# Kernel tuning notes

Hardware: AMD Instinct MI355X
Metric: run time of the kernel (lower is better)

Reference implementation:

```python
import jax, jax.numpy as jnp
import numpy as np

N_PER_GRAPH = 468
B = 32
N = B * N_PER_GRAPH            # 14976 nodes
E = 89600                      # synthetic Delaunay-like directed edges
IN_DIM, HID, OUT, HEADS = 2, 256, 512, 4
NEG_SLOPE = 0.2
EPS = 1e-16


def setup_inputs() -> dict:
    key = jax.random.key(0)
    ks = jax.random.split(key, 12)
    x = jax.random.uniform(ks[0], (N, IN_DIM), dtype=jnp.float32)
    edge_index = jax.random.randint(ks[1], (2, E), 0, N, dtype=jnp.int64)
    batch = jnp.repeat(jnp.arange(B, dtype=jnp.int64), N_PER_GRAPH)
    s1 = 1.0 / np.sqrt(IN_DIM)
    s2 = 1.0 / np.sqrt(HID)
    sg = 1.0 / np.sqrt(OUT)
    return {
        "x": x,
        "edge_index": edge_index,
        "batch": batch,
        # GATConv 1: in_dim -> hidden, heads=4, concat=False
        "W1": jax.random.normal(ks[2], (IN_DIM, HEADS * HID), jnp.float32) * s1,
        "a1_src": jax.random.normal(ks[3], (HEADS, HID), jnp.float32) * s2,
        "a1_dst": jax.random.normal(ks[4], (HEADS, HID), jnp.float32) * s2,
        "b1": jnp.zeros((HID,), jnp.float32),
        # GATConv 2: hidden -> out, heads=4, concat=False
        "W2": jax.random.normal(ks[5], (HID, HEADS * OUT), jnp.float32) * s2,
        "a2_src": jax.random.normal(ks[6], (HEADS, OUT), jnp.float32) * sg,
        "a2_dst": jax.random.normal(ks[7], (HEADS, OUT), jnp.float32) * sg,
        "b2": jnp.zeros((OUT,), jnp.float32),
        # GlobalAttention gate_nn: Linear(out_dim, 1)
        "Wg": jax.random.normal(ks[8], (OUT, 1), jnp.float32) * sg,
        "bg": jnp.zeros((1,), jnp.float32),
    }


def _gat_layer(x, src, dst, W, a_src, a_dst, b, heads, out_ch):
    n = x.shape[0]
    xh = (x @ W).reshape(n, heads, out_ch)            # [N,H,C]
    alpha_s = jnp.einsum("nhc,hc->nh", xh, a_src)     # [N,H]
    alpha_d = jnp.einsum("nhc,hc->nh", xh, a_dst)
    e = alpha_s[src] + alpha_d[dst]                   # [E,H]
    e = jnp.where(e > 0, e, NEG_SLOPE * e)            # leaky_relu(0.2)
    # segment softmax over incoming edges of each destination node
    m = jax.ops.segment_max(e, dst, num_segments=n)
    ex = jnp.exp(e - m[dst])
    denom = jax.ops.segment_sum(ex, dst, num_segments=n)
    alpha = ex / (denom[dst] + EPS)                   # [E,H]
    msg = xh[src] * alpha[:, :, None]                 # [E,H,C]
    out = jax.ops.segment_sum(msg, dst, num_segments=n)  # [N,H,C]
    return out.mean(axis=1) + b                       # concat=False -> head mean


def reference(x, edge_index, batch, W1, a1_src, a1_dst, b1,
              W2, a2_src, a2_dst, b2, Wg, bg):
    n = x.shape[0]
    # PyG GATConv default add_self_loops=True (both layers use the same graph)
    loops = jnp.arange(n, dtype=edge_index.dtype)
    src = jnp.concatenate([edge_index[0], loops])
    dst = jnp.concatenate([edge_index[1], loops])

    h = _gat_layer(x, src, dst, W1, a1_src, a1_dst, b1, HEADS, HID)
    h = jax.nn.relu(h)
    h = _gat_layer(h, src, dst, W2, a2_src, a2_dst, b2, HEADS, OUT)
    h = jax.nn.relu(h)

    # GlobalAttention pooling: gate = Linear(out,1), softmax per graph, weighted sum
    gate = h @ Wg + bg                                # [N,1]
    gm = jax.ops.segment_max(gate, batch, num_segments=B)
    ge = jnp.exp(gate - gm[batch])
    gs = jax.ops.segment_sum(ge, batch, num_segments=B)
    attn = ge / (gs[batch] + EPS)                     # [N,1]
    pooled = jax.ops.segment_sum(attn * h, batch, num_segments=B)  # [B,512]
    return pooled.reshape(-1, 1, OUT)                 # [B,1,512]
```

## Files before the change

kernel.cpp:

```cpp
#include <hip/hip_runtime.h>
#include <hip/hip_bf16.h>
#include <math.h>

#define HEADS 4
#define C1 256
#define C2 512
#define NEG 0.2f
#define EPSF 1e-16f

using bf16x8 = __attribute__((ext_vector_type(8))) short;
using f32x4  = __attribute__((ext_vector_type(4))) float;

__device__ __forceinline__ float lrelu(float e) { return e > 0.f ? e : NEG * e; }

__device__ __forceinline__ unsigned short f2bf(float v) {
    __hip_bfloat16 b = __float2bfloat16(v);
    return *reinterpret_cast<unsigned short*>(&b);
}
__device__ __forceinline__ float bf2f(unsigned short u) {
    __hip_bfloat16 b = *reinterpret_cast<__hip_bfloat16*>(&u);
    return __bfloat162float(b);
}


__global__ __launch_bounds__(256) void k1_prep_deg(
    const float* __restrict__ W1, const float* __restrict__ a1s, const float* __restrict__ a1d,
    const float* __restrict__ W2, const float* __restrict__ a2s, const float* __restrict__ a2d,
    const int* __restrict__ ei, int E,
    float* __restrict__ w1a, float* __restrict__ w2a,
    unsigned short* __restrict__ W2t_hi, unsigned short* __restrict__ W2t_lo,
    int* __restrict__ deg)
{
    int b = blockIdx.x, tid = threadIdx.x;
    int wv = tid >> 6, lane = tid & 63;
    if (b == 0) {
#pragma unroll
        for (int q = 0; q < 4; q++) {
            int o = wv * 4 + q, sd = o >> 3, idx = o & 7, h = idx >> 1, d = idx & 1;
            const float* av = sd ? a1d : a1s;
            float p = 0.f;
            for (int c = lane; c < 256; c += 64) p += W1[d * 1024 + h * 256 + c] * av[h * 256 + c];
#pragma unroll
            for (int m = 32; m >= 1; m >>= 1) p += __shfl_xor(p, m, 64);
            if (lane == 0) w1a[o] = p;
        }
    } else if (b <= 8) {
        int bb = b - 1, sd = bb >> 2, h = bb & 3;
        const float* av = sd ? a2d : a2s;
        float gv[8];
#pragma unroll
        for (int q = 0; q < 8; q++) gv[q] = av[h * 512 + lane * 8 + q];
        for (int k = wv; k < 256; k += 4) {
            const float4 w0 = *reinterpret_cast<const float4*>(&W2[(size_t)k * 2048 + h * 512 + lane * 8]);
            const float4 w1 = *reinterpret_cast<const float4*>(&W2[(size_t)k * 2048 + h * 512 + lane * 8 + 4]);
            float p = w0.x*gv[0] + w0.y*gv[1] + w0.z*gv[2] + w0.w*gv[3]
                    + w1.x*gv[4] + w1.y*gv[5] + w1.z*gv[6] + w1.w*gv[7];
#pragma unroll
            for (int m = 32; m >= 1; m >>= 1) p += __shfl_xor(p, m, 64);
            if (lane == 0) w2a[sd * 1024 + h * 256 + k] = p;
        }
    } else if (b <= 136) {
        __shared__ float T[64][65];
        int lin = b - 9;
        int kk0 = (lin & 15) * 64, n0 = (lin >> 4) * 64;
        int h = kk0 >> 8, k0 = kk0 & 255;
#pragma unroll
        for (int rr = 0; rr < 16; rr++) {
            int ki = rr * 4 + (tid >> 6), ni = tid & 63;
            T[ki][ni] = W2[(size_t)(k0 + ki) * 2048 + h * 512 + n0 + ni];
        }
        __syncthreads();
#pragma unroll
        for (int rr = 0; rr < 16; rr++) {
            int ni = rr * 4 + (tid >> 6), ki = tid & 63;
            float v = T[ki][ni];
            unsigned short hi = f2bf(v);
            unsigned short lo = f2bf(v - bf2f(hi));
            size_t o = (size_t)(n0 + ni) * 1024 + kk0 + ki;
            W2t_hi[o] = hi; W2t_lo[o] = lo;
        }
    } else {
        int i = (b - 137) * 256 + tid;
        if (i < E) atomicAdd(&deg[ei[E + i]], 1);
    }
}

__global__ __launch_bounds__(1024) void k2_node1_scan(
    const float* __restrict__ x, const float* __restrict__ w1a,
    float* __restrict__ as1, float* __restrict__ ad1, int N,
    const int* __restrict__ deg, int* __restrict__ row_ptr, int* __restrict__ cursor)
{
    int b = blockIdx.x, tid = threadIdx.x;
    if (b < 15) {
        int n = b * 1024 + tid;
        if (n >= N) return;
        float x0 = x[2 * n], x1 = x[2 * n + 1];
        float4 av, dv;
        float* ap = &av.x; float* dp = &dv.x;
#pragma unroll
        for (int h = 0; h < 4; h++) {
            ap[h] = x0 * w1a[h * 2] + x1 * w1a[h * 2 + 1];
            dp[h] = x0 * w1a[8 + h * 2] + x1 * w1a[8 + h * 2 + 1];
        }
        *reinterpret_cast<float4*>(&as1[n * 4]) = av;
        *reinterpret_cast<float4*>(&ad1[n * 4]) = dv;
    } else {
        __shared__ int sd[1024];
        int per = (N + 1023) >> 10;
        int vals[24];
        int start = tid * per, local = 0;
        for (int i = 0; i < per && i < 24; i++) {
            int idx = start + i;
            int d = (idx < N) ? deg[idx] : 0;
            vals[i] = d; local += d;
        }
        sd[tid] = local; __syncthreads();
        for (int off = 1; off < 1024; off <<= 1) {
            int v = sd[tid];
            int a = (tid >= off) ? sd[tid - off] : 0;
            __syncthreads();
            sd[tid] = v + a;
            __syncthreads();
        }
        int run = (tid > 0) ? sd[tid - 1] : 0;
        for (int i = 0; i < per && i < 24; i++) {
            int idx = start + i;
            if (idx < N) { row_ptr[idx] = run; cursor[idx] = run; run += vals[i]; }
        }
        if (tid == 1023) row_ptr[N] = sd[1023];
    }
}

__global__ void k3_scatter(const int* __restrict__ ei, int E,
                           int* __restrict__ cursor, int* __restrict__ csr_src)
{
    int i = blockIdx.x * blockDim.x + threadIdx.x;
    if (i >= E) return;
    int s = ei[i], d = ei[E + i];
    int pos = atomicAdd(&cursor[d], 1);
    csr_src[pos] = s;
}

__global__ __launch_bounds__(256) void k4_agg1_h1(
    const float* __restrict__ x, const float* __restrict__ as1, const float* __restrict__ ad1,
    const int* __restrict__ row_ptr, const int* __restrict__ csr_src,
    const float* __restrict__ W1, const float* __restrict__ b1, const float* __restrict__ w2a,
    float* __restrict__ h1, float* __restrict__ as2, float* __restrict__ ad2)
{
    int wv = threadIdx.x >> 6, lane = threadIdx.x & 63;
    int n = blockIdx.x * 4 + wv;
    const float4 sa4 = *reinterpret_cast<const float4*>(&as1[n * 4]);
    const float4 da4 = *reinterpret_cast<const float4*>(&ad1[n * 4]);
    const float sa[4] = {sa4.x, sa4.y, sa4.z, sa4.w};
    const float da[4] = {da4.x, da4.y, da4.z, da4.w};
    float acc[8] = {0,0,0,0,0,0,0,0};
    float den[4] = {0,0,0,0};
    int beg = row_ptr[n], end = row_ptr[n + 1];
    for (int e = beg + lane; e < end; e += 64) {
        int s = csr_src[e];
        const float4 a4 = *reinterpret_cast<const float4*>(&as1[s * 4]);
        const float af[4] = {a4.x, a4.y, a4.z, a4.w};
        const float2 xv = reinterpret_cast<const float2*>(x)[s];
#pragma unroll
        for (int q = 0; q < 4; q++) {
            float w = expf(lrelu(af[q] + da[q]));
            den[q] += w;
            acc[2 * q]     = fmaf(w, xv.x, acc[2 * q]);
            acc[2 * q + 1] = fmaf(w, xv.y, acc[2 * q + 1]);
        }
    }
#pragma unroll
    for (int msk = 1; msk <= 32; msk <<= 1) {
#pragma unroll
        for (int q = 0; q < 8; q++) acc[q] += __shfl_xor(acc[q], msk, 64);
#pragma unroll
        for (int q = 0; q < 4; q++) den[q] += __shfl_xor(den[q], msk, 64);
    }
    const float2 xn = reinterpret_cast<const float2*>(x)[n];
    float xa[8];
#pragma unroll
    for (int q = 0; q < 4; q++) {
        float ws = expf(lrelu(sa[q] + da[q]));
        float dq = den[q] + ws;
        float inv = 1.f / (dq + EPSF);
        xa[2 * q]     = (acc[2 * q]     + ws * xn.x) * inv;
        xa[2 * q + 1] = (acc[2 * q + 1] + ws * xn.y) * inv;
    }
    float v[4];
#pragma unroll
    for (int q = 0; q < 4; q++) {
        int c = lane * 4 + q;
        float t = 0.f;
#pragma unroll
        for (int h = 0; h < 4; h++)
#pragma unroll
            for (int d = 0; d < 2; d++)
                t = fmaf(xa[h * 2 + d], W1[d * 1024 + h * 256 + c], t);
        v[q] = fmaxf(fmaf(0.25f, t, b1[c]), 0.f);
    }
    *reinterpret_cast<float4*>(&h1[(size_t)n * 256 + lane * 4]) = make_float4(v[0], v[1], v[2], v[3]);
    float p[8];
#pragma unroll
    for (int o = 0; o < 8; o++) {
        int sd = o >> 2, h = o & 3;
        float t = 0.f;
#pragma unroll
        for (int q = 0; q < 4; q++) t = fmaf(v[q], w2a[sd * 1024 + h * 256 + lane * 4 + q], t);
        p[o] = t;
    }
#pragma unroll
    for (int msk = 1; msk <= 32; msk <<= 1)
#pragma unroll
        for (int o = 0; o < 8; o++) p[o] += __shfl_xor(p[o], msk, 64);
    if (lane == 0) {
        *reinterpret_cast<float4*>(&as2[n * 4]) = make_float4(p[0], p[1], p[2], p[3]);
        *reinterpret_cast<float4*>(&ad2[n * 4]) = make_float4(p[4], p[5], p[6], p[7]);
    }
}

__global__ __launch_bounds__(256) void k6_agg2(
    const float* __restrict__ h1, const float* __restrict__ as2, const float* __restrict__ ad2,
    const int* __restrict__ row_ptr, const int* __restrict__ csr_src,
    unsigned short* __restrict__ hagg_hi, unsigned short* __restrict__ hagg_lo)
{
    int wv = threadIdx.x >> 6, lane = threadIdx.x & 63;
    int n = blockIdx.x * 4 + wv;
    const float4 sa4 = *reinterpret_cast<const float4*>(&as2[n * 4]);
    const float4 da4 = *reinterpret_cast<const float4*>(&ad2[n * 4]);
    const float sa[4] = {sa4.x, sa4.y, sa4.z, sa4.w};
    const float da[4] = {da4.x, da4.y, da4.z, da4.w};
    float den[4], acc[4][4];
    const float4 hs = *reinterpret_cast<const float4*>(&h1[(size_t)n * 256 + lane * 4]);
    const float hv0[4] = {hs.x, hs.y, hs.z, hs.w};
#pragma unroll
    for (int h = 0; h < 4; h++) {
        float ws = expf(lrelu(sa[h] + da[h]));
        den[h] = ws;
#pragma unroll
        for (int q = 0; q < 4; q++) acc[h][q] = ws * hv0[q];
    }
    int beg = row_ptr[n], end = row_ptr[n + 1];
    for (int e = beg; e < end; e++) {
        int s = csr_src[e];
        const float4 a4 = *reinterpret_cast<const float4*>(&as2[s * 4]);
        const float af[4] = {a4.x, a4.y, a4.z, a4.w};
        const float4 hv = *reinterpret_cast<const float4*>(&h1[(size_t)s * 256 + lane * 4]);
#pragma unroll
        for (int h = 0; h < 4; h++) {
            float w = expf(lrelu(af[h] + da[h]));
            den[h] += w;
            acc[h][0] = fmaf(w, hv.x, acc[h][0]);
            acc[h][1] = fmaf(w, hv.y, acc[h][1]);
            acc[h][2] = fmaf(w, hv.z, acc[h][2]);
            acc[h][3] = fmaf(w, hv.w, acc[h][3]);
        }
    }
#pragma unroll
    for (int h = 0; h < 4; h++) {
        float inv = 1.f / (den[h] + EPSF);
        ushort4 hi4, lo4;
        unsigned short* hp = &hi4.x; unsigned short* lp = &lo4.x;
#pragma unroll
        for (int q = 0; q < 4; q++) {
            float val = acc[h][q] * inv;
            unsigned short hi = f2bf(val);
            hp[q] = hi;
            lp[q] = f2bf(val - bf2f(hi));
        }
        size_t o = (size_t)n * 1024 + h * 256 + lane * 4;
        *reinterpret_cast<ushort4*>(&hagg_hi[o]) = hi4;
        *reinterpret_cast<ushort4*>(&hagg_lo[o]) = lo4;
    }
}

__global__ __launch_bounds__(256) void k7_gemm2(
    const unsigned short* __restrict__ Ahi, const unsigned short* __restrict__ Alo,
    const unsigned short* __restrict__ Bhi, const unsigned short* __restrict__ Blo,
    const float* __restrict__ b2, const float* __restrict__ Wg,
    float* __restrict__ h2, float* __restrict__ gate)
{
    __shared__ __align__(16) unsigned short As_hi[128 * 40], As_lo[128 * 40];
    __shared__ __align__(16) unsigned short Bs_hi[64 * 40],  Bs_lo[64 * 40];
    __shared__ float s_gate[128];
    int tid = threadIdx.x, l = tid & 63, wv = tid >> 6;
    int wr = wv >> 1, wc = wv & 1;
    int bid = blockIdx.x, rtile, ctile;
    if (bid < 896) { int g = bid >> 6, rem = bid & 63; rtile = g * 8 + (rem & 7); ctile = rem >> 3; }
    else           { int t = bid - 896; rtile = 112 + (t >> 3); ctile = t & 7; }
    int row0 = rtile * 128, col0 = ctile * 64;
    int lm = l & 15, lg = l >> 4;
    if (tid < 128) s_gate[tid] = 0.f;

    int ra0 = tid >> 2, ka0 = (tid & 3) * 8;
    int ra1 = (tid + 256) >> 2, ka1 = ((tid + 256) & 3) * 8;
    int rb = tid >> 2, kb = (tid & 3) * 8;

    f32x4 acc[4][2];
#pragma unroll
    for (int i = 0; i < 4; i++)
#pragma unroll
        for (int j = 0; j < 2; j++) { acc[i][j][0]=0.f; acc[i][j][1]=0.f; acc[i][j][2]=0.f; acc[i][j][3]=0.f; }

    uint4 pah0, pah1, pal0, pal1, pbh, pbl;
    {
        size_t ga0 = (size_t)(row0 + ra0) * 1024 + ka0;
        size_t ga1 = (size_t)(row0 + ra1) * 1024 + ka1;
        size_t gb  = (size_t)(col0 + rb) * 1024 + kb;
        pah0 = *reinterpret_cast<const uint4*>(Ahi + ga0); pal0 = *reinterpret_cast<const uint4*>(Alo + ga0);
        pah1 = *reinterpret_cast<const uint4*>(Ahi + ga1); pal1 = *reinterpret_cast<const uint4*>(Alo + ga1);
        pbh  = *reinterpret_cast<const uint4*>(Bhi + gb);  pbl  = *reinterpret_cast<const uint4*>(Blo + gb);
    }

    for (int kt = 0; kt < 1024; kt += 32) {
        *reinterpret_cast<uint4*>(&As_hi[ra0 * 40 + ka0]) = pah0;
        *reinterpret_cast<uint4*>(&As_lo[ra0 * 40 + ka0]) = pal0;
        *reinterpret_cast<uint4*>(&As_hi[ra1 * 40 + ka1]) = pah1;
        *reinterpret_cast<uint4*>(&As_lo[ra1 * 40 + ka1]) = pal1;
        *reinterpret_cast<uint4*>(&Bs_hi[rb * 40 + kb])   = pbh;
        *reinterpret_cast<uint4*>(&Bs_lo[rb * 40 + kb])   = pbl;
        __syncthreads();
        if (kt + 32 < 1024) {
            int ktn = kt + 32;
            size_t ga0 = (size_t)(row0 + ra0) * 1024 + ktn + ka0;
            size_t ga1 = (size_t)(row0 + ra1) * 1024 + ktn + ka1;
            size_t gb  = (size_t)(col0 + rb) * 1024 + ktn + kb;
            pah0 = *reinterpret_cast<const uint4*>(Ahi + ga0); pal0 = *reinterpret_cast<const uint4*>(Alo + ga0);
            pah1 = *reinterpret_cast<const uint4*>(Ahi + ga1); pal1 = *reinterpret_cast<const uint4*>(Alo + ga1);
            pbh  = *reinterpret_cast<const uint4*>(Bhi + gb);  pbl  = *reinterpret_cast<const uint4*>(Blo + gb);
        }
        bf16x8 ah[4], al[4], bh[2], bl[2];
#pragma unroll
        for (int i = 0; i < 4; i++) {
            int base = (wr * 64 + i * 16 + lm) * 40 + lg * 8;
            ah[i] = *reinterpret_cast<const bf16x8*>(&As_hi[base]);
            al[i] = *reinterpret_cast<const bf16x8*>(&As_lo[base]);
        }
#pragma unroll
        for (int j = 0; j < 2; j++) {
            int base = (wc * 32 + j * 16 + lm) * 40 + lg * 8;
            bh[j] = *reinterpret_cast<const bf16x8*>(&Bs_hi[base]);
            bl[j] = *reinterpret_cast<const bf16x8*>(&Bs_lo[base]);
        }
#pragma unroll
        for (int i = 0; i < 4; i++)
#pragma unroll
            for (int j = 0; j < 2; j++) {
                acc[i][j] = __builtin_amdgcn_mfma_f32_16x16x32_bf16(ah[i], bh[j], acc[i][j], 0, 0, 0);
                acc[i][j] = __builtin_amdgcn_mfma_f32_16x16x32_bf16(ah[i], bl[j], acc[i][j], 0, 0, 0);
                acc[i][j] = __builtin_amdgcn_mfma_f32_16x16x32_bf16(al[i], bh[j], acc[i][j], 0, 0, 0);
            }
        __syncthreads();
    }
    float b2c[2], wgj[2];
#pragma unroll
    for (int j = 0; j < 2; j++) {
        int col = col0 + wc * 32 + j * 16 + lm;
        b2c[j] = b2[col]; wgj[j] = Wg[col];
    }
#pragma unroll
    for (int i = 0; i < 4; i++) {
#pragma unroll
        for (int r = 0; r < 4; r++) {
            int row = row0 + wr * 64 + i * 16 + lg * 4 + r;
            float g = 0.f;
#pragma unroll
            for (int j = 0; j < 2; j++) {
                float v = fmaxf(fmaf(0.25f, acc[i][j][r], b2c[j]), 0.f);
                h2[(size_t)row * 512 + col0 + wc * 32 + j * 16 + lm] = v;
                g = fmaf(v, wgj[j], g);
            }
            g += __shfl_xor(g, 1, 64);
            g += __shfl_xor(g, 2, 64);
            g += __shfl_xor(g, 4, 64);
            g += __shfl_xor(g, 8, 64);
            if (lm == 0) atomicAdd(&s_gate[wr * 64 + i * 16 + lg * 4 + r], g);
        }
    }
    __syncthreads();
    if (tid < 128) atomicAdd(&gate[row0 + tid], s_gate[tid]);
}

__global__ __launch_bounds__(256) void k8a_stats(float* __restrict__ gate, int npg)
{
    int bq = blockIdx.x, tid = threadIdx.x;
    int n0 = bq * npg;
    __shared__ float s[256];
    float e0 = (tid < npg)       ? expf(gate[n0 + tid])       : 0.f;
    float e1 = (tid + 256 < npg) ? expf(gate[n0 + tid + 256]) : 0.f;
    s[tid] = e0 + e1; __syncthreads();
#pragma unroll
    for (int off = 128; off >= 1; off >>= 1) {
        if (tid < off) s[tid] += s[tid + off];
        __syncthreads();
    }
    float inv = 1.f / (s[0] + EPSF);
    if (tid < npg)       gate[n0 + tid]       = e0 * inv;
    if (tid + 256 < npg) gate[n0 + tid + 256] = e1 * inv;
}

__global__ __launch_bounds__(256) void k8b_pool(
    const float* __restrict__ attn, const float* __restrict__ h2,
    float* __restrict__ out, int npg, int nsplit)
{
    int bq = blockIdx.x, sp = blockIdx.y, tid = threadIdx.x;
    int slot = tid & 127, half = tid >> 7;
    int chunk = (npg + nsplit - 1) / nsplit;
    int i0 = sp * chunk, i1 = min(npg, i0 + chunk);
    int n0 = bq * npg;
    float4 acc = make_float4(0.f, 0.f, 0.f, 0.f);
    for (int i = i0 + half; i < i1; i += 2) {
        float w = attn[n0 + i];
        const float4 v = *reinterpret_cast<const float4*>(&h2[(size_t)(n0 + i) * 512 + slot * 4]);
        acc.x = fmaf(w, v.x, acc.x);
        acc.y = fmaf(w, v.y, acc.y);
        acc.z = fmaf(w, v.z, acc.z);
        acc.w = fmaf(w, v.w, acc.w);
    }
    __shared__ float4 sacc[128];
    if (half == 1) sacc[slot] = acc;
    __syncthreads();
    if (half == 0) {
        const float4 o = sacc[slot];
        float* op = &out[(size_t)bq * 512 + slot * 4];
        atomicAdd(op + 0, acc.x + o.x);
        atomicAdd(op + 1, acc.y + o.y);
        atomicAdd(op + 2, acc.z + o.z);
        atomicAdd(op + 3, acc.w + o.w);
    }
}

extern "C" void kernel_launch(void* const* d_in, const int* in_sizes, int n_in,
                              void* d_out, int out_size, void* d_ws, size_t ws_size,
                              hipStream_t stream)
{
    const float* x    = (const float*)d_in[0];
    const int*   ei   = (const int*)d_in[1];
    const float* W1   = (const float*)d_in[3];
    const float* a1s  = (const float*)d_in[4];
    const float* a1d  = (const float*)d_in[5];
    const float* b1   = (const float*)d_in[6];
    const float* W2   = (const float*)d_in[7];
    const float* a2s  = (const float*)d_in[8];
    const float* a2d  = (const float*)d_in[9];
    const float* b2   = (const float*)d_in[10];
    const float* Wg   = (const float*)d_in[11];
    float* out = (float*)d_out;

    const int N = in_sizes[0] / 2;
    const int E = in_sizes[1] / 2;
    const int Bq = out_size / C2;
    const int npg = N / Bq;

    char* w = (char*)d_ws;
    size_t off = 0;
    auto alloc = [&](size_t bytes) { void* p = w + off; off += (bytes + 255) & ~(size_t)255; return p; };

    float* h1       = (float*)alloc((size_t)N * 256 * 4);
    float* h2       = (float*)alloc((size_t)N * 512 * 4);
    unsigned short* hagg_hi = (unsigned short*)alloc((size_t)N * 1024 * 2);
    unsigned short* hagg_lo = (unsigned short*)alloc((size_t)N * 1024 * 2);
    unsigned short* W2t_hi  = (unsigned short*)alloc((size_t)512 * 1024 * 2);
    unsigned short* W2t_lo  = (unsigned short*)alloc((size_t)512 * 1024 * 2);
    float* as1   = (float*)alloc((size_t)N * 4 * 4);
    float* ad1   = (float*)alloc((size_t)N * 4 * 4);
    float* as2   = (float*)alloc((size_t)N * 4 * 4);
    float* ad2   = (float*)alloc((size_t)N * 4 * 4);
    int*   deg   = (int*)alloc((size_t)N * 4);
    float* gate  = (float*)alloc((size_t)N * 4);
    float* w1a   = (float*)alloc(16 * 4);
    float* w2a   = (float*)alloc(2048 * 4);
    int* row_ptr = (int*)alloc((size_t)(N + 1) * 4);
    int* cursor  = (int*)alloc((size_t)(N + 1) * 4);
    int* csr_src = (int*)alloc((size_t)E * 4);
    (void)ws_size; (void)n_in;

    const int EB = (E + 255) / 256;

    hipMemsetAsync(deg, 0, (size_t)N * 4 * 2, stream);
    hipMemsetAsync(out, 0, (size_t)out_size * 4, stream);

    k1_prep_deg<<<137 + EB, 256, 0, stream>>>(W1, a1s, a1d, W2, a2s, a2d, ei, E,
                                              w1a, w2a, W2t_hi, W2t_lo, deg);
    k2_node1_scan<<<16, 1024, 0, stream>>>(x, w1a, as1, ad1, N, deg, row_ptr, cursor);
    k3_scatter<<<EB, 256, 0, stream>>>(ei, E, cursor, csr_src);
    k4_agg1_h1<<<N / 4, 256, 0, stream>>>(x, as1, ad1, row_ptr, csr_src,
                                          W1, b1, w2a, h1, as2, ad2);
    k6_agg2<<<N / 4, 256, 0, stream>>>(h1, as2, ad2, row_ptr, csr_src, hagg_hi, hagg_lo);
    k7_gemm2<<<(N / 128) * 8, 256, 0, stream>>>(hagg_hi, hagg_lo, W2t_hi, W2t_lo,
                                                b2, Wg, h2, gate);
    k8a_stats<<<Bq, 256, 0, stream>>>(gate, npg);
    k8b_pool<<<dim3(Bq, 8), 256, 0, stream>>>(gate, h2, out, npg, 8);
}
```

Baseline: 281.1 us.

## Widen GEMM2 column tile to 128 and fuse pooling softmax with weighted sum

The second-layer GEMM now computes 128x128 output tiles per block instead of 128x64, so each A tile is loaded once for twice as many columns and the grid halves to 468 blocks. The gate softmax statistics and the attention-weighted pooling are merged into one kernel that writes outputs directly, which removes the output memset and the atomics. The larger tile doubles the accumulator registers and LDS use, which may lower occupancy, and the pooling kernel now launches fewer blocks.

```diff
diff --git a/kernel.cpp b/kernel.cpp
--- a/kernel.cpp
+++ b/kernel.cpp
@@ -280,55 +280,56 @@
     float* __restrict__ h2, float* __restrict__ gate)
 {
     __shared__ __align__(16) unsigned short As_hi[128 * 40], As_lo[128 * 40];
-    __shared__ __align__(16) unsigned short Bs_hi[64 * 40],  Bs_lo[64 * 40];
+    __shared__ __align__(16) unsigned short Bs_hi[128 * 40], Bs_lo[128 * 40];
     __shared__ float s_gate[128];
     int tid = threadIdx.x, l = tid & 63, wv = tid >> 6;
     int wr = wv >> 1, wc = wv & 1;
     int bid = blockIdx.x, rtile, ctile;
-    if (bid < 896) { int g = bid >> 6, rem = bid & 63; rtile = g * 8 + (rem & 7); ctile = rem >> 3; }
-    else           { int t = bid - 896; rtile = 112 + (t >> 3); ctile = t & 7; }
-    int row0 = rtile * 128, col0 = ctile * 64;
+    if (bid < 448) { rtile = (bid & 7) + 8 * (bid >> 5); ctile = (bid >> 3) & 3; }
+    else           { int t = bid - 448; rtile = 112 + (t >> 2); ctile = t & 3; }
+    int row0 = rtile * 128, col0 = ctile * 128;
     int lm = l & 15, lg = l >> 4;
     if (tid < 128) s_gate[tid] = 0.f;
 
-    int ra0 = tid >> 2, ka0 = (tid & 3) * 8;
-    int ra1 = (tid + 256) >> 2, ka1 = ((tid + 256) & 3) * 8;
-    int rb = tid >> 2, kb = (tid & 3) * 8;
-
-    f32x4 acc[4][2];
+    int r0 = tid >> 2, k00 = (tid & 3) * 8;
+    int r1 = (tid + 256) >> 2, k01 = ((tid + 256) & 3) * 8;
+
+    f32x4 acc[4][4];
 #pragma unroll
     for (int i = 0; i < 4; i++)
 #pragma unroll
-        for (int j = 0; j < 2; j++) { acc[i][j][0]=0.f; acc[i][j][1]=0.f; acc[i][j][2]=0.f; acc[i][j][3]=0.f; }
-
-    uint4 pah0, pah1, pal0, pal1, pbh, pbl;
+        for (int jj = 0; jj < 4; jj++) { acc[i][jj][0]=0.f; acc[i][jj][1]=0.f; acc[i][jj][2]=0.f; acc[i][jj][3]=0.f; }
+
+    uint4 pah0, pal0, pbh0, pbl0, pah1, pal1, pbh1, pbl1;
     {
-        size_t ga0 = (size_t)(row0 + ra0) * 1024 + ka0;
-        size_t ga1 = (size_t)(row0 + ra1) * 1024 + ka1;
-        size_t gb  = (size_t)(col0 + rb) * 1024 + kb;
+        size_t ga0 = (size_t)(row0 + r0) * 1024 + k00, gb0 = (size_t)(col0 + r0) * 1024 + k00;
+        size_t ga1 = (size_t)(row0 + r1) * 1024 + k01, gb1 = (size_t)(col0 + r1) * 1024 + k01;
         pah0 = *reinterpret_cast<const uint4*>(Ahi + ga0); pal0 = *reinterpret_cast<const uint4*>(Alo + ga0);
+        pbh0 = *reinterpret_cast<const uint4*>(Bhi + gb0); pbl0 = *reinterpret_cast<const uint4*>(Blo + gb0);
         pah1 = *reinterpret_cast<const uint4*>(Ahi + ga1); pal1 = *reinterpret_cast<const uint4*>(Alo + ga1);
-        pbh  = *reinterpret_cast<const uint4*>(Bhi + gb);  pbl  = *reinterpret_cast<const uint4*>(Blo + gb);
+        pbh1 = *reinterpret_cast<const uint4*>(Bhi + gb1); pbl1 = *reinterpret_cast<const uint4*>(Blo + gb1);
     }
 
     for (int kt = 0; kt < 1024; kt += 32) {
-        *reinterpret_cast<uint4*>(&As_hi[ra0 * 40 + ka0]) = pah0;
-        *reinterpret_cast<uint4*>(&As_lo[ra0 * 40 + ka0]) = pal0;
-        *reinterpret_cast<uint4*>(&As_hi[ra1 * 40 + ka1]) = pah1;
-        *reinterpret_cast<uint4*>(&As_lo[ra1 * 40 + ka1]) = pal1;
-        *reinterpret_cast<uint4*>(&Bs_hi[rb * 40 + kb])   = pbh;
-        *reinterpret_cast<uint4*>(&Bs_lo[rb * 40 + kb])   = pbl;
+        *reinterpret_cast<uint4*>(&As_hi[r0 * 40 + k00]) = pah0;
+        *reinterpret_cast<uint4*>(&As_lo[r0 * 40 + k00]) = pal0;
+        *reinterpret_cast<uint4*>(&Bs_hi[r0 * 40 + k00]) = pbh0;
+        *reinterpret_cast<uint4*>(&Bs_lo[r0 * 40 + k00]) = pbl0;
+        *reinterpret_cast<uint4*>(&As_hi[r1 * 40 + k01]) = pah1;
+        *reinterpret_cast<uint4*>(&As_lo[r1 * 40 + k01]) = pal1;
+        *reinterpret_cast<uint4*>(&Bs_hi[r1 * 40 + k01]) = pbh1;
+        *reinterpret_cast<uint4*>(&Bs_lo[r1 * 40 + k01]) = pbl1;
         __syncthreads();
         if (kt + 32 < 1024) {
             int ktn = kt + 32;
-            size_t ga0 = (size_t)(row0 + ra0) * 1024 + ktn + ka0;
-            size_t ga1 = (size_t)(row0 + ra1) * 1024 + ktn + ka1;
-            size_t gb  = (size_t)(col0 + rb) * 1024 + ktn + kb;
+            size_t ga0 = (size_t)(row0 + r0) * 1024 + ktn + k00, gb0 = (size_t)(col0 + r0) * 1024 + ktn + k00;
+            size_t ga1 = (size_t)(row0 + r1) * 1024 + ktn + k01, gb1 = (size_t)(col0 + r1) * 1024 + ktn + k01;
             pah0 = *reinterpret_cast<const uint4*>(Ahi + ga0); pal0 = *reinterpret_cast<const uint4*>(Alo + ga0);
+            pbh0 = *reinterpret_cast<const uint4*>(Bhi + gb0); pbl0 = *reinterpret_cast<const uint4*>(Blo + gb0);
             pah1 = *reinterpret_cast<const uint4*>(Ahi + ga1); pal1 = *reinterpret_cast<const uint4*>(Alo + ga1);
-            pbh  = *reinterpret_cast<const uint4*>(Bhi + gb);  pbl  = *reinterpret_cast<const uint4*>(Blo + gb);
-        }
-        bf16x8 ah[4], al[4], bh[2], bl[2];
+            pbh1 = *reinterpret_cast<const uint4*>(Bhi + gb1); pbl1 = *reinterpret_cast<const uint4*>(Blo + gb1);
+        }
+        bf16x8 ah[4], al[4], bh[4], bl[4];
 #pragma unroll
         for (int i = 0; i < 4; i++) {
             int base = (wr * 64 + i * 16 + lm) * 40 + lg * 8;
@@ -336,26 +337,26 @@
             al[i] = *reinterpret_cast<const bf16x8*>(&As_lo[base]);
         }
 #pragma unroll
-        for (int j = 0; j < 2; j++) {
-            int base = (wc * 32 + j * 16 + lm) * 40 + lg * 8;
-            bh[j] = *reinterpret_cast<const bf16x8*>(&Bs_hi[base]);
-            bl[j] = *reinterpret_cast<const bf16x8*>(&Bs_lo[base]);
+        for (int jj = 0; jj < 4; jj++) {
+            int base = (wc * 64 + jj * 16 + lm) * 40 + lg * 8;
+            bh[jj] = *reinterpret_cast<const bf16x8*>(&Bs_hi[base]);
+            bl[jj] = *reinterpret_cast<const bf16x8*>(&Bs_lo[base]);
         }
 #pragma unroll
         for (int i = 0; i < 4; i++)
 #pragma unroll
-            for (int j = 0; j < 2; j++) {
-                acc[i][j] = __builtin_amdgcn_mfma_f32_16x16x32_bf16(ah[i], bh[j], acc[i][j], 0, 0, 0);
-                acc[i][j] = __builtin_amdgcn_mfma_f32_16x16x32_bf16(ah[i], bl[j], acc[i][j], 0, 0, 0);
-                acc[i][j] = __builtin_amdgcn_mfma_f32_16x16x32_bf16(al[i], bh[j], acc[i][j], 0, 0, 0);
+            for (int jj = 0; jj < 4; jj++) {
+                acc[i][jj] = __builtin_amdgcn_mfma_f32_16x16x32_bf16(ah[i], bh[jj], acc[i][jj], 0, 0, 0);
+                acc[i][jj] = __builtin_amdgcn_mfma_f32_16x16x32_bf16(ah[i], bl[jj], acc[i][jj], 0, 0, 0);
+                acc[i][jj] = __builtin_amdgcn_mfma_f32_16x16x32_bf16(al[i], bh[jj], acc[i][jj], 0, 0, 0);
             }
         __syncthreads();
     }
-    float b2c[2], wgj[2];
-#pragma unroll
-    for (int j = 0; j < 2; j++) {
-        int col = col0 + wc * 32 + j * 16 + lm;
-        b2c[j] = b2[col]; wgj[j] = Wg[col];
+    float b2c[4], wgj[4];
+#pragma unroll
+    for (int jj = 0; jj < 4; jj++) {
+        int col = col0 + wc * 64 + jj * 16 + lm;
+        b2c[jj] = b2[col]; wgj[jj] = Wg[col];
     }
 #pragma unroll
     for (int i = 0; i < 4; i++) {
@@ -364,10 +365,10 @@
             int row = row0 + wr * 64 + i * 16 + lg * 4 + r;
             float g = 0.f;
 #pragma unroll
-            for (int j = 0; j < 2; j++) {
-                float v = fmaxf(fmaf(0.25f, acc[i][j][r], b2c[j]), 0.f);
-                h2[(size_t)row * 512 + col0 + wc * 32 + j * 16 + lm] = v;
-                g = fmaf(v, wgj[j], g);
+            for (int jj = 0; jj < 4; jj++) {
+                float v = fmaxf(fmaf(0.25f, acc[i][jj][r], b2c[jj]), 0.f);
+                h2[(size_t)row * 512 + col0 + wc * 64 + jj * 16 + lm] = v;
+                g = fmaf(v, wgj[jj], g);
             }
             g += __shfl_xor(g, 1, 64);
             g += __shfl_xor(g, 2, 64);
@@ -380,52 +381,47 @@
     if (tid < 128) atomicAdd(&gate[row0 + tid], s_gate[tid]);
 }
 
-__global__ __launch_bounds__(256) void k8a_stats(float* __restrict__ gate, int npg)
-{
-    int bq = blockIdx.x, tid = threadIdx.x;
+__global__ __launch_bounds__(256) void k8_pool(
+    const float* __restrict__ gate, const float* __restrict__ h2,
+    float* __restrict__ out, int npg)
+{
+    int bq = blockIdx.x, cs = blockIdx.y, tid = threadIdx.x;
     int n0 = bq * npg;
-    __shared__ float s[256];
-    float e0 = (tid < npg)       ? expf(gate[n0 + tid])       : 0.f;
-    float e1 = (tid + 256 < npg) ? expf(gate[n0 + tid + 256]) : 0.f;
-    s[tid] = e0 + e1; __syncthreads();
-#pragma unroll
-    for (int off = 128; off >= 1; off >>= 1) {
-        if (tid < off) s[tid] += s[tid + off];
-        __syncthreads();
-    }
-    float inv = 1.f / (s[0] + EPSF);
-    if (tid < npg)       gate[n0 + tid]       = e0 * inv;
-    if (tid + 256 < npg) gate[n0 + tid + 256] = e1 * inv;
-}
-
-__global__ __launch_bounds__(256) void k8b_pool(
-    const float* __restrict__ attn, const float* __restrict__ h2,
-    float* __restrict__ out, int npg, int nsplit)
-{
-    int bq = blockIdx.x, sp = blockIdx.y, tid = threadIdx.x;
-    int slot = tid & 127, half = tid >> 7;
-    int chunk = (npg + nsplit - 1) / nsplit;
-    int i0 = sp * chunk, i1 = min(npg, i0 + chunk);
-    int n0 = bq * npg;
+    __shared__ float sw[512];
+    __shared__ float sred[4];
+    __shared__ float4 sacc[256];
+    float part = 0.f;
+    for (int i = tid; i < 512; i += 256) {
+        float e = (i < npg) ? expf(gate[n0 + i]) : 0.f;
+        sw[i] = e; part += e;
+    }
+#pragma unroll
+    for (int m = 32; m >= 1; m >>= 1) part += __shfl_xor(part, m, 64);
+    if ((tid & 63) == 0) sred[tid >> 6] = part;
+    __syncthreads();
+    float inv = 1.f / (sred[0] + sred[1] + sred[2] + sred[3] + EPSF);
+    int slot = tid & 31, sub = tid >> 5;
+    const float* base = h2 + (size_t)n0 * 512 + cs * 128 + slot * 4;
     float4 acc = make_float4(0.f, 0.f, 0.f, 0.f);
-    for (int i = i0 + half; i < i1; i += 2) {
-        float w = attn[n0 + i];
-        const float4 v = *reinterpret_cast<const float4*>(&h2[(size_t)(n0 + i) * 512 + slot * 4]);
+    for (int i = sub; i < npg; i += 8) {
+        float w = sw[i];
+        const float4 v = *reinterpret_cast<const float4*>(base + (size_t)i * 512);
         acc.x = fmaf(w, v.x, acc.x);
         acc.y = fmaf(w, v.y, acc.y);
         acc.z = fmaf(w, v.z, acc.z);
         acc.w = fmaf(w, v.w, acc.w);
     }
-    __shared__ float4 sacc[128];
-    if (half == 1) sacc[slot] = acc;
+    sacc[tid] = acc;
     __syncthreads();
-    if (half == 0) {
-        const float4 o = sacc[slot];
-        float* op = &out[(size_t)bq * 512 + slot * 4];
-        atomicAdd(op + 0, acc.x + o.x);
-        atomicAdd(op + 1, acc.y + o.y);
-        atomicAdd(op + 2, acc.z + o.z);
-        atomicAdd(op + 3, acc.w + o.w);
+    if (sub == 0) {
+        float4 t = acc;
+#pragma unroll
+        for (int s2 = 1; s2 < 8; s2++) {
+            const float4 o = sacc[s2 * 32 + slot];
+            t.x += o.x; t.y += o.y; t.z += o.z; t.w += o.w;
+        }
+        t.x *= inv; t.y *= inv; t.z *= inv; t.w *= inv;
+        *reinterpret_cast<float4*>(&out[(size_t)bq * 512 + cs * 128 + slot * 4]) = t;
     }
 }
 
@@ -477,7 +473,6 @@
     const int EB = (E + 255) / 256;
 
     hipMemsetAsync(deg, 0, (size_t)N * 4 * 2, stream);
-    hipMemsetAsync(out, 0, (size_t)out_size * 4, stream);
 
     k1_prep_deg<<<137 + EB, 256, 0, stream>>>(W1, a1s, a1d, W2, a2s, a2d, ei, E,
                                               w1a, w2a, W2t_hi, W2t_lo, deg);
@@ -486,8 +481,7 @@
     k4_agg1_h1<<<N / 4, 256, 0, stream>>>(x, as1, ad1, row_ptr, csr_src,
                                           W1, b1, w2a, h1, as2, ad2);
     k6_agg2<<<N / 4, 256, 0, stream>>>(h1, as2, ad2, row_ptr, csr_src, hagg_hi, hagg_lo);
-    k7_gemm2<<<(N / 128) * 8, 256, 0, stream>>>(hagg_hi, hagg_lo, W2t_hi, W2t_lo,
-                                                b2, Wg, h2, gate);
-    k8a_stats<<<Bq, 256, 0, stream>>>(gate, npg);
-    k8b_pool<<<dim3(Bq, 8), 256, 0, stream>>>(gate, h2, out, npg, 8);
-}
+    k7_gemm2<<<468, 256, 0, stream>>>(hagg_hi, hagg_lo, W2t_hi, W2t_lo,
+                                      b2, Wg, h2, gate);
+    k8_pool<<<dim3(Bq, 4), 256, 0, stream>>>(gate, h2, out, npg);
+}
```

Measured after the change: 276.9 us. Within noise of the previous version (-1.5%).
